# Optimization experiments

Hardware: AMD Instinct MI355X
Metric: run time of the kernel (lower is better)

Reference implementation:

```python
import jax, jax.numpy as jnp
import numpy as np


def _build_transform():
    # Deterministic re-creation of SegmentationAugmentation.build_3d_transform
    # with flip=True, offset=0.1, scale=0.2, rotate=True.
    rng = np.random.default_rng(0)
    t = np.eye(4, dtype=np.float32)
    for i in range(3):
        if rng.random() > 0.5:
            t[i, i] *= -1.0
        t[i, 3] = 0.1 * (rng.random() * 2.0 - 1.0)
        t[i, i] *= 1.0 + 0.2 * (rng.random() * 2.0 - 1.0)
    a = rng.random() * 2.0 * np.pi
    s, c = np.sin(a), np.cos(a)
    rot = np.array([[c, -s, 0, 0], [s, c, 0, 0], [0, 0, 1, 0], [0, 0, 0, 1]],
                   dtype=np.float32)
    return t @ rot


def _affine_grid(theta, size):
    # theta: [B,3,4]; size: (B,C,D,H,W); align_corners=False.
    B, C, D, H, W = size
    def lin(n):
        # pixel-center normalized coords: (2i+1)/n - 1
        return (2.0 * jnp.arange(n, dtype=jnp.float32) + 1.0) / n - 1.0
    z, y, x = jnp.meshgrid(lin(D), lin(H), lin(W), indexing='ij')
    pts = jnp.stack([x, y, z], axis=-1)  # [D,H,W,3], (x,y,z) order as in torch
    return (jnp.einsum('bij,dhwj->bdhwi', theta[:, :, :3], pts)
            + theta[:, None, None, None, :, 3])


def _grid_sample_3d_border(inp, grid):
    # trilinear grid_sample, padding_mode='border', align_corners=False.
    # inp: [B,C,D,H,W]; grid: [B,Do,Ho,Wo,3] with (x,y,z) normalized coords.
    B, C, D, H, W = inp.shape
    Do, Ho, Wo = grid.shape[1:4]

    def unnorm(cn, n):
        # align_corners=False unnormalize, then border clamp
        return jnp.clip(((cn + 1.0) * n - 1.0) * 0.5, 0.0, n - 1.0)

    x = unnorm(grid[..., 0], W)
    y = unnorm(grid[..., 1], H)
    z = unnorm(grid[..., 2], D)
    x0 = jnp.floor(x); y0 = jnp.floor(y); z0 = jnp.floor(z)
    fx, fy, fz = x - x0, y - y0, z - z0
    x0i = x0.astype(jnp.int32); y0i = y0.astype(jnp.int32); z0i = z0.astype(jnp.int32)
    x1i = jnp.minimum(x0i + 1, W - 1)
    y1i = jnp.minimum(y0i + 1, H - 1)
    z1i = jnp.minimum(z0i + 1, D - 1)

    inp_flat = inp.reshape(B, C, D * H * W)
    N = Do * Ho * Wo
    out = jnp.zeros((B, C, N), dtype=inp.dtype)
    for zi, wz in ((z0i, 1.0 - fz), (z1i, fz)):
        for yi, wy in ((y0i, 1.0 - fy), (y1i, fy)):
            for xi, wx in ((x0i, 1.0 - fx), (x1i, fx)):
                idx = ((zi * H + yi) * W + xi).reshape(B, 1, N)
                v = jnp.take_along_axis(
                    inp_flat, jnp.broadcast_to(idx, (B, C, N)), axis=2)
                w = (wz * wy * wx).reshape(B, 1, N)
                out = out + v * w
    return out.reshape(B, C, Do, Ho, Wo)


def setup_inputs() -> dict:
    key = jax.random.key(0)
    k1, k2 = jax.random.split(key)
    input_g = jax.random.normal(k1, (8, 1, 128, 128, 128), dtype=jnp.float32)
    label_g = jax.random.uniform(k2, (8, 1, 128, 128, 128), dtype=jnp.float32)
    transform = jnp.asarray(_build_transform())
    return {"input_g": input_g, "label_g": label_g, "transform": transform}


def reference(input_g, label_g, transform):
    # transpose(-3,-1): swap depth and width axes
    inp = jnp.swapaxes(input_g, -3, -1)
    lab = jnp.swapaxes(label_g, -3, -1)
    B = inp.shape[0]
    theta = jnp.broadcast_to(transform[:3][None], (B, 3, 4)).astype(jnp.float32)
    grid = _affine_grid(theta, inp.shape)
    aug_inp = _grid_sample_3d_border(inp, grid)
    aug_lab = _grid_sample_3d_border(lab, grid)
    aug_inp = jnp.swapaxes(aug_inp, -3, -1)
    aug_lab = jnp.swapaxes(aug_lab, -3, -1)
    return aug_inp, aug_lab > 0.5
```

## Files before the change

kernel.cpp:

```cpp
#include <hip/hip_runtime.h>


#define NV 128
#define TOTAL (8 * NV * NV * NV)

__global__ __launch_bounds__(128) void rowparam_kernel(
    const float* __restrict__ T, float4* __restrict__ rp)
{
#pragma clang fp contract(off)
    const int idx = blockIdx.x * 128 + threadIdx.x;
    const int o3 = idx & (NV - 1);
    const int o2 = idx >> 7;

    float p2 = (2.0f * (float)o2 + 1.0f) / 128.0f - 1.0f;
    float p3 = (2.0f * (float)o3 + 1.0f) / 128.0f - 1.0f;
    float ux = (T[0] * p2 + T[1] * p3) + T[3];
    float uy = (T[4] * p2 + T[5] * p3) + T[7];
    float gx = ((ux + 1.0f) * 128.0f - 1.0f) * 0.5f;
    float gy = ((uy + 1.0f) * 128.0f - 1.0f) * 0.5f;
    gx = fminf(fmaxf(gx, 0.0f), 127.0f);
    gy = fminf(fmaxf(gy, 0.0f), 127.0f);
    float fx0f = floorf(gx), fy0f = floorf(gy);
    float fx = gx - fx0f;
    float fy = gy - fy0f;
    int ix0 = (int)fx0f, iy0 = (int)fy0f;
    int ix1 = min(ix0 + 1, NV - 1);
    int iy1 = min(iy0 + 1, NV - 1);

    float4 ri, rw;
    ri.x = __int_as_float((ix0 * NV + iy0) * NV);
    ri.y = __int_as_float((ix0 * NV + iy1) * NV);
    ri.z = __int_as_float((ix1 * NV + iy0) * NV);
    ri.w = __int_as_float((ix1 * NV + iy1) * NV);
    rw.x = 1.0f - fx;  rw.y = fx;
    rw.z = 1.0f - fy;  rw.w = fy;
    rp[2 * idx] = ri;
    rp[2 * idx + 1] = rw;
}

__global__ __launch_bounds__(128) void seg_aug_kernel(
    const float* __restrict__ in,
    const float* __restrict__ lab,
    const float* __restrict__ T,
    const float4* __restrict__ rp,
    float* __restrict__ out_in,
    float* __restrict__ out_lab)
{
#pragma clang fp contract(off)
    __shared__ float s[8 * NV];

    const int t = threadIdx.x;
    const int row = blockIdx.x & 16383;
    const int b = blockIdx.x >> 14;

    const float4 ri = rp[2 * row];
    const float4 rw = rp[2 * row + 1];
    const int r00 = __builtin_amdgcn_readfirstlane(__float_as_int(ri.x));
    const int r01 = __builtin_amdgcn_readfirstlane(__float_as_int(ri.y));
    const int r10 = __builtin_amdgcn_readfirstlane(__float_as_int(ri.z));
    const int r11 = __builtin_amdgcn_readfirstlane(__float_as_int(ri.w));
    const float wx0 = rw.x, wx1 = rw.y, wy0 = rw.z, wy1 = rw.w;

    const size_t bbase = (size_t)b << 21;
    const float* ibp = in  + bbase;
    const float* lbp = lab + bbase;
    {
        const int rid = t >> 5;
        const int seg = t & 31;
        int rb = (rid & 2) ? ((rid & 1) ? r11 : r10)
                           : ((rid & 1) ? r01 : r00);
        const int off = rb + seg * 4;
        __builtin_amdgcn_global_load_lds(ibp + off, &s[t * 4],       16, 0, 0);
        __builtin_amdgcn_global_load_lds(lbp + off, &s[512 + t * 4], 16, 0, 0);
    }

    float p4 = (2.0f * (float)t + 1.0f) / 128.0f - 1.0f;
    float uz = T[10] * p4 + T[11];
    float gz = ((uz + 1.0f) * 128.0f - 1.0f) * 0.5f;
    gz = fminf(fmaxf(gz, 0.0f), 127.0f);
    float fz0f = floorf(gz);
    float fz = gz - fz0f;
    int iz0 = (int)fz0f;
    float wz0 = 1.0f - fz, wz1 = fz;

    const int zb = min(iz0, NV - 2);
    const bool hi = (iz0 == NV - 1);

    __syncthreads();

    #define PAIR(ROW, A, B)                                       \
        float A, B;                                               \
        {                                                         \
            float2 _p;                                            \
            __builtin_memcpy(&_p, &s[(ROW) * NV + zb], 8);        \
            A = _p.x; B = _p.y;                                   \
        }

    PAIR(0, ia00, ib00)
    PAIR(1, ia01, ib01)
    PAIR(2, ia10, ib10)
    PAIR(3, ia11, ib11)
    PAIR(4, la00, lb00)
    PAIR(5, la01, lb01)
    PAIR(6, la10, lb10)
    PAIR(7, la11, lb11)
    #undef PAIR

    float vi000 = hi ? ib00 : ia00;
    float vi010 = hi ? ib01 : ia01;
    float vi100 = hi ? ib10 : ia10;
    float vi110 = hi ? ib11 : ia11;
    float vl000 = hi ? lb00 : la00;
    float vl010 = hi ? lb01 : la01;
    float vl100 = hi ? lb10 : la10;
    float vl110 = hi ? lb11 : la11;

    float tz0y0 = wz0 * wy0, tz0y1 = wz0 * wy1;
    float tz1y0 = wz1 * wy0, tz1y1 = wz1 * wy1;
    float w1 = tz0y0 * wx0, w2 = tz0y0 * wx1;
    float w3 = tz0y1 * wx0, w4 = tz0y1 * wx1;
    float w5 = tz1y0 * wx0, w6 = tz1y0 * wx1;
    float w7 = tz1y1 * wx0, w8 = tz1y1 * wx1;

    float acc_i = 0.0f;
    acc_i = acc_i + vi000 * w1;
    acc_i = acc_i + vi100 * w2;
    acc_i = acc_i + vi010 * w3;
    acc_i = acc_i + vi110 * w4;
    acc_i = acc_i + ib00 * w5;
    acc_i = acc_i + ib10 * w6;
    acc_i = acc_i + ib01 * w7;
    acc_i = acc_i + ib11 * w8;

    float acc_l = 0.0f;
    acc_l = acc_l + vl000 * w1;
    acc_l = acc_l + vl100 * w2;
    acc_l = acc_l + vl010 * w3;
    acc_l = acc_l + vl110 * w4;
    acc_l = acc_l + lb00 * w5;
    acc_l = acc_l + lb10 * w6;
    acc_l = acc_l + lb01 * w7;
    acc_l = acc_l + lb11 * w8;

    const int oidx = blockIdx.x * NV + t;
    out_in[oidx]  = acc_i;
    out_lab[oidx] = (acc_l > 0.5f) ? 1.0f : 0.0f;
}

extern "C" void kernel_launch(void* const* d_in, const int* in_sizes, int n_in,
                              void* d_out, int out_size, void* d_ws, size_t ws_size,
                              hipStream_t stream) {
    const float* in  = (const float*)d_in[0];
    const float* lab = (const float*)d_in[1];
    const float* T   = (const float*)d_in[2];
    float* out_in  = (float*)d_out;
    float* out_lab = (float*)d_out + TOTAL;
    float4* rp = (float4*)d_ws;

    rowparam_kernel<<<128, 128, 0, stream>>>(T, rp);
    seg_aug_kernel<<<TOTAL / 128, 128, 0, stream>>>(in, lab, T, rp,
                                                    out_in, out_lab);
}
```

Measured before the change: 250.0 us.

## Make seg_aug waves persistent over 16 rows with two outputs per lane

```diff
diff --git a/kernel.cpp b/kernel.cpp
--- a/kernel.cpp
+++ b/kernel.cpp
@@ -2,7 +2,10 @@
 
 
 #define NV 128
-#define TOTAL (8 * NV * NV * NV)
+#define NROWS (8 * NV * NV)
+#define TOTAL (NROWS * NV)
+#define NBLK 2048
+#define RPW 16
 
 __global__ __launch_bounds__(128) void rowparam_kernel(
     const float* __restrict__ T, float4* __restrict__ rp)
@@ -38,7 +41,7 @@
     rp[2 * idx + 1] = rw;
 }
 
-__global__ __launch_bounds__(128) void seg_aug_kernel(
+__global__ __launch_bounds__(256) void seg_aug_kernel(
     const float* __restrict__ in,
     const float* __restrict__ lab,
     const float* __restrict__ T,
@@ -47,104 +50,158 @@
     float* __restrict__ out_lab)
 {
 #pragma clang fp contract(off)
-    __shared__ float s[8 * NV];
-
-    const int t = threadIdx.x;
-    const int row = blockIdx.x & 16383;
-    const int b = blockIdx.x >> 14;
-
-    const float4 ri = rp[2 * row];
-    const float4 rw = rp[2 * row + 1];
-    const int r00 = __builtin_amdgcn_readfirstlane(__float_as_int(ri.x));
-    const int r01 = __builtin_amdgcn_readfirstlane(__float_as_int(ri.y));
-    const int r10 = __builtin_amdgcn_readfirstlane(__float_as_int(ri.z));
-    const int r11 = __builtin_amdgcn_readfirstlane(__float_as_int(ri.w));
-    const float wx0 = rw.x, wx1 = rw.y, wy0 = rw.z, wy1 = rw.w;
-
-    const size_t bbase = (size_t)b << 21;
-    const float* ibp = in  + bbase;
-    const float* lbp = lab + bbase;
+    __shared__ float s[4 * 8 * NV];
+    const int lane = threadIdx.x & 63;
+    const int wid  = threadIdx.x >> 6;
+    float* sw = &s[wid * (8 * NV)];
+
+    float wz0A, wz1A, wz0B, wz1B;
+    int zbA, zbB;
+    bool hiA, hiB;
     {
-        const int rid = t >> 5;
-        const int seg = t & 31;
-        int rb = (rid & 2) ? ((rid & 1) ? r11 : r10)
-                           : ((rid & 1) ? r01 : r00);
-        const int off = rb + seg * 4;
-        __builtin_amdgcn_global_load_lds(ibp + off, &s[t * 4],       16, 0, 0);
-        __builtin_amdgcn_global_load_lds(lbp + off, &s[512 + t * 4], 16, 0, 0);
+        float p4 = (2.0f * (float)lane + 1.0f) / 128.0f - 1.0f;
+        float uz = T[10] * p4 + T[11];
+        float gz = ((uz + 1.0f) * 128.0f - 1.0f) * 0.5f;
+        gz = fminf(fmaxf(gz, 0.0f), 127.0f);
+        float f0 = floorf(gz);
+        float fz = gz - f0;
+        int iz0 = (int)f0;
+        wz0A = 1.0f - fz; wz1A = fz;
+        zbA = min(iz0, NV - 2);
+        hiA = (iz0 == NV - 1);
     }
-
-    float p4 = (2.0f * (float)t + 1.0f) / 128.0f - 1.0f;
-    float uz = T[10] * p4 + T[11];
-    float gz = ((uz + 1.0f) * 128.0f - 1.0f) * 0.5f;
-    gz = fminf(fmaxf(gz, 0.0f), 127.0f);
-    float fz0f = floorf(gz);
-    float fz = gz - fz0f;
-    int iz0 = (int)fz0f;
-    float wz0 = 1.0f - fz, wz1 = fz;
-
-    const int zb = min(iz0, NV - 2);
-    const bool hi = (iz0 == NV - 1);
-
-    __syncthreads();
-
-    #define PAIR(ROW, A, B)                                       \
-        float A, B;                                               \
-        {                                                         \
-            float2 _p;                                            \
-            __builtin_memcpy(&_p, &s[(ROW) * NV + zb], 8);        \
-            A = _p.x; B = _p.y;                                   \
-        }
-
-    PAIR(0, ia00, ib00)
-    PAIR(1, ia01, ib01)
-    PAIR(2, ia10, ib10)
-    PAIR(3, ia11, ib11)
-    PAIR(4, la00, lb00)
-    PAIR(5, la01, lb01)
-    PAIR(6, la10, lb10)
-    PAIR(7, la11, lb11)
-    #undef PAIR
-
-    float vi000 = hi ? ib00 : ia00;
-    float vi010 = hi ? ib01 : ia01;
-    float vi100 = hi ? ib10 : ia10;
-    float vi110 = hi ? ib11 : ia11;
-    float vl000 = hi ? lb00 : la00;
-    float vl010 = hi ? lb01 : la01;
-    float vl100 = hi ? lb10 : la10;
-    float vl110 = hi ? lb11 : la11;
-
-    float tz0y0 = wz0 * wy0, tz0y1 = wz0 * wy1;
-    float tz1y0 = wz1 * wy0, tz1y1 = wz1 * wy1;
-    float w1 = tz0y0 * wx0, w2 = tz0y0 * wx1;
-    float w3 = tz0y1 * wx0, w4 = tz0y1 * wx1;
-    float w5 = tz1y0 * wx0, w6 = tz1y0 * wx1;
-    float w7 = tz1y1 * wx0, w8 = tz1y1 * wx1;
-
-    float acc_i = 0.0f;
-    acc_i = acc_i + vi000 * w1;
-    acc_i = acc_i + vi100 * w2;
-    acc_i = acc_i + vi010 * w3;
-    acc_i = acc_i + vi110 * w4;
-    acc_i = acc_i + ib00 * w5;
-    acc_i = acc_i + ib10 * w6;
-    acc_i = acc_i + ib01 * w7;
-    acc_i = acc_i + ib11 * w8;
-
-    float acc_l = 0.0f;
-    acc_l = acc_l + vl000 * w1;
-    acc_l = acc_l + vl100 * w2;
-    acc_l = acc_l + vl010 * w3;
-    acc_l = acc_l + vl110 * w4;
-    acc_l = acc_l + lb00 * w5;
-    acc_l = acc_l + lb10 * w6;
-    acc_l = acc_l + lb01 * w7;
-    acc_l = acc_l + lb11 * w8;
-
-    const int oidx = blockIdx.x * NV + t;
-    out_in[oidx]  = acc_i;
-    out_lab[oidx] = (acc_l > 0.5f) ? 1.0f : 0.0f;
+    {
+        float p4 = (2.0f * (float)(lane + 64) + 1.0f) / 128.0f - 1.0f;
+        float uz = T[10] * p4 + T[11];
+        float gz = ((uz + 1.0f) * 128.0f - 1.0f) * 0.5f;
+        gz = fminf(fmaxf(gz, 0.0f), 127.0f);
+        float f0 = floorf(gz);
+        float fz = gz - f0;
+        int iz0 = (int)f0;
+        wz0B = 1.0f - fz; wz1B = fz;
+        zbB = min(iz0, NV - 2);
+        hiB = (iz0 == NV - 1);
+    }
+
+    const int gw = blockIdx.x * 4 + wid;
+    const int rbeg = gw * RPW;
+
+    for (int r = rbeg; r < rbeg + RPW; ++r) {
+        const int row = r & (NROWS / 8 - 1);
+        const size_t bbase = (size_t)(r >> 14) << 21;
+        const float* ibp = in  + bbase;
+        const float* lbp = lab + bbase;
+
+        const float4 ri = rp[2 * row];
+        const float4 rw = rp[2 * row + 1];
+        const int r00 = __float_as_int(ri.x);
+        const int r01 = __float_as_int(ri.y);
+        const int r10 = __float_as_int(ri.z);
+        const int r11 = __float_as_int(ri.w);
+        const float wx0 = rw.x, wx1 = rw.y, wy0 = rw.z, wy1 = rw.w;
+
+        const int seg = (lane & 31) * 4;
+        const int s0 = ((lane & 32) ? r01 : r00) + seg;
+        const int s1 = ((lane & 32) ? r11 : r10) + seg;
+        __builtin_amdgcn_global_load_lds(ibp + s0, sw + lane * 4,       16, 0, 0);
+        __builtin_amdgcn_global_load_lds(ibp + s1, sw + 256 + lane * 4, 16, 0, 0);
+        __builtin_amdgcn_global_load_lds(lbp + s0, sw + 512 + lane * 4, 16, 0, 0);
+        __builtin_amdgcn_global_load_lds(lbp + s1, sw + 768 + lane * 4, 16, 0, 0);
+
+        asm volatile("s_waitcnt vmcnt(0)" ::: "memory");
+
+        #define PAIRR(OFF, PA, PB)                                \
+            float2 PA, PB;                                        \
+            __builtin_memcpy(&PA, sw + (OFF) + zbA, 8);           \
+            __builtin_memcpy(&PB, sw + (OFF) + zbB, 8);
+        PAIRR(0,   i00A, i00B)
+        PAIRR(128, i01A, i01B)
+        PAIRR(256, i10A, i10B)
+        PAIRR(384, i11A, i11B)
+        PAIRR(512, l00A, l00B)
+        PAIRR(640, l01A, l01B)
+        PAIRR(768, l10A, l10B)
+        PAIRR(896, l11A, l11B)
+        #undef PAIRR
+
+        float vi000 = hiA ? i00A.y : i00A.x;
+        float vi010 = hiA ? i01A.y : i01A.x;
+        float vi100 = hiA ? i10A.y : i10A.x;
+        float vi110 = hiA ? i11A.y : i11A.x;
+        float vl000 = hiA ? l00A.y : l00A.x;
+        float vl010 = hiA ? l01A.y : l01A.x;
+        float vl100 = hiA ? l10A.y : l10A.x;
+        float vl110 = hiA ? l11A.y : l11A.x;
+
+        float tz0y0 = wz0A * wy0, tz0y1 = wz0A * wy1;
+        float tz1y0 = wz1A * wy0, tz1y1 = wz1A * wy1;
+        float w1 = tz0y0 * wx0, w2 = tz0y0 * wx1;
+        float w3 = tz0y1 * wx0, w4 = tz0y1 * wx1;
+        float w5 = tz1y0 * wx0, w6 = tz1y0 * wx1;
+        float w7 = tz1y1 * wx0, w8 = tz1y1 * wx1;
+
+        float accAi = 0.0f;
+        accAi = accAi + vi000 * w1;
+        accAi = accAi + vi100 * w2;
+        accAi = accAi + vi010 * w3;
+        accAi = accAi + vi110 * w4;
+        accAi = accAi + i00A.y * w5;
+        accAi = accAi + i10A.y * w6;
+        accAi = accAi + i01A.y * w7;
+        accAi = accAi + i11A.y * w8;
+
+        float accAl = 0.0f;
+        accAl = accAl + vl000 * w1;
+        accAl = accAl + vl100 * w2;
+        accAl = accAl + vl010 * w3;
+        accAl = accAl + vl110 * w4;
+        accAl = accAl + l00A.y * w5;
+        accAl = accAl + l10A.y * w6;
+        accAl = accAl + l01A.y * w7;
+        accAl = accAl + l11A.y * w8;
+
+        float ui000 = hiB ? i00B.y : i00B.x;
+        float ui010 = hiB ? i01B.y : i01B.x;
+        float ui100 = hiB ? i10B.y : i10B.x;
+        float ui110 = hiB ? i11B.y : i11B.x;
+        float ul000 = hiB ? l00B.y : l00B.x;
+        float ul010 = hiB ? l01B.y : l01B.x;
+        float ul100 = hiB ? l10B.y : l10B.x;
+        float ul110 = hiB ? l11B.y : l11B.x;
+
+        float sz0y0 = wz0B * wy0, sz0y1 = wz0B * wy1;
+        float sz1y0 = wz1B * wy0, sz1y1 = wz1B * wy1;
+        float v1 = sz0y0 * wx0, v2 = sz0y0 * wx1;
+        float v3 = sz0y1 * wx0, v4 = sz0y1 * wx1;
+        float v5 = sz1y0 * wx0, v6 = sz1y0 * wx1;
+        float v7 = sz1y1 * wx0, v8 = sz1y1 * wx1;
+
+        float accBi = 0.0f;
+        accBi = accBi + ui000 * v1;
+        accBi = accBi + ui100 * v2;
+        accBi = accBi + ui010 * v3;
+        accBi = accBi + ui110 * v4;
+        accBi = accBi + i00B.y * v5;
+        accBi = accBi + i10B.y * v6;
+        accBi = accBi + i01B.y * v7;
+        accBi = accBi + i11B.y * v8;
+
+        float accBl = 0.0f;
+        accBl = accBl + ul000 * v1;
+        accBl = accBl + ul100 * v2;
+        accBl = accBl + ul010 * v3;
+        accBl = accBl + ul110 * v4;
+        accBl = accBl + l00B.y * v5;
+        accBl = accBl + l10B.y * v6;
+        accBl = accBl + l01B.y * v7;
+        accBl = accBl + l11B.y * v8;
+
+        const int ob = r * NV + lane;
+        out_in[ob]       = accAi;
+        out_in[ob + 64]  = accBi;
+        out_lab[ob]      = (accAl > 0.5f) ? 1.0f : 0.0f;
+        out_lab[ob + 64] = (accBl > 0.5f) ? 1.0f : 0.0f;
+    }
 }
 
 extern "C" void kernel_launch(void* const* d_in, const int* in_sizes, int n_in,
@@ -158,6 +215,5 @@
     float4* rp = (float4*)d_ws;
 
     rowparam_kernel<<<128, 128, 0, stream>>>(T, rp);
-    seg_aug_kernel<<<TOTAL / 128, 128, 0, stream>>>(in, lab, T, rp,
-                                                    out_in, out_lab);
+    seg_aug_kernel<<<NBLK, 256, 0, stream>>>(in, lab, T, rp, out_in, out_lab);
 }
```

After: 285.7 us. 1.14x slower.
